# Optimization experiments

Hardware: AMD Instinct MI355X
Metric: run time of the kernel (lower is better)

## Reference

```python
import jax, jax.numpy as jnp
import numpy as np

# config (matches init_kwargs)
B, H, N, D = 2, 8, 2048, 64
ALPHA = 1.0        # < 2 -> power-law kernel branch
D_INT = 4.0        # d_intrinsic
BW = 1.0           # bandwidth
A = 0.5            # dual-sided degree-normalization exponent
R = 1.0            # sphere_radius
MASK_VAL = 10000.0
EPS = 1e-7


def setup_inputs() -> dict:
    key = jax.random.key(0)
    k1, k2, k3, k4 = jax.random.split(key, 4)
    Q = jax.random.normal(k1, (B, H, N, D), dtype=jnp.float32)
    K = jax.random.normal(k2, (B, H, N, D), dtype=jnp.float32)
    V = jax.random.normal(k3, (B, H, N, D), dtype=jnp.float32)
    mask = jax.random.randint(k4, (B, N), 0, 2).astype(jnp.int32)
    return {"Q": Q, "K": K, "V": V, "mask": mask}


def reference(Q, K, V, mask) -> jnp.ndarray:
    # geodesic distance on the sphere: acos(clamp(QK^T)) * radius  [B,H,N,N]
    qk = jnp.einsum('bhnd,bhmd->bhnm', Q, K)
    g_dist = jnp.arccos(jnp.clip(qk, -1.0 + EPS, 1.0 - EPS)) * R
    # key-side padding mask: [B,N] -> [B,1,1,N]
    g_dist = jnp.where(mask[:, None, None, :] == 0, MASK_VAL, g_dist)
    # power-law kernel (alpha < 2 branch)
    attn_score = (1.0 + g_dist / jnp.sqrt(BW)) ** (-D_INT - ALPHA)
    # dual-sided degree normalization (a != 0 branch)
    n_r = jnp.sum(attn_score, axis=-1)   # row degrees [B,H,N]
    n_c = jnp.sum(attn_score, axis=-2)   # col degrees [B,H,N]
    k_tilde = (n_r ** (-A))[..., :, None] * attn_score * (n_c ** (-A))[..., None, :]
    # F.normalize(p=1, dim=3)
    attn = k_tilde / jnp.maximum(jnp.sum(jnp.abs(k_tilde), axis=-1, keepdims=True), 1e-12)
    # dropout p=0.0 -> identity
    return jnp.einsum('bhnm,bhmd->bhnd', attn, V)
```

## Files before the change

### kernel.cpp

```cpp
#include <hip/hip_runtime.h>
#include <hip/hip_bf16.h>
#include <math.h>

#define B_ 2
#define H_ 8
#define N_ 2048
#define D_ 64
#define BH_ 16
#define NT_ (N_/64)
#define LS 72
#define LSW (LS/2)

typedef __attribute__((ext_vector_type(8))) short short8;
typedef __attribute__((ext_vector_type(4))) float float4v;
typedef __attribute__((ext_vector_type(2))) float float2v;

__device__ __forceinline__ float2v splat2(float s){ float2v v; v.x=s; v.y=s; return v; }

__device__ __forceinline__ unsigned packbf2(float a, float b){
  __hip_bfloat162 h = __float22bfloat162_rn(make_float2(a, b));
  return *(unsigned*)&h;
}
__device__ __forceinline__ void split2(float a, float b, unsigned& hi, unsigned& lo){
  hi = packbf2(a, b);
  float ha = __uint_as_float(hi << 16);
  float hb = __uint_as_float(hi & 0xFFFF0000u);
  lo = packbf2(a - ha, b - hb);
}
__device__ __forceinline__ void load_split8(const float* p, short8& hi8, short8& lo8){
  float4v v0 = *(const float4v*)p;
  float4v v1 = *(const float4v*)(p + 4);
  unsigned h0,h1,h2,h3,l0,l1,l2,l3;
  split2(v0.x, v0.y, h0, l0);
  split2(v0.z, v0.w, h1, l1);
  split2(v1.x, v1.y, h2, l2);
  split2(v1.z, v1.w, h3, l3);
  unsigned ph[4] = {h0,h1,h2,h3};
  unsigned pl[4] = {l0,l1,l2,l3};
  hi8 = *(short8*)ph;
  lo8 = *(short8*)pl;
}

__device__ __forceinline__ float2v score2(float2v qk){
  float2v ax;
  ax.x = fminf(fabsf(qk.x), 1.0f - 1e-7f);
  ax.y = fminf(fabsf(qk.y), 1.0f - 1e-7f);
  float2v p = __builtin_elementwise_fma(
                __builtin_elementwise_fma(
                  __builtin_elementwise_fma(splat2(-0.0187293f), ax, splat2(0.0742610f)),
                  ax, splat2(-0.2121144f)),
                ax, splat2(1.5707288f));
  float2v u = __builtin_elementwise_fma(ax, splat2(-1.0f), splat2(1.0f));
  float2v t;
  t.x = __builtin_amdgcn_sqrtf(u.x);
  t.y = __builtin_amdgcn_sqrtf(u.y);
  float2v t2 = t * p;
  float2v gn = __builtin_elementwise_fma(t2, splat2(-1.0f), splat2(3.14159265358979f));
  float2v g;
  g.x = (qk.x >= 0.0f) ? t2.x : gn.x;
  g.y = (qk.y >= 0.0f) ? t2.y : gn.y;
  float2v w1 = g + splat2(1.0f);
  float2v w2 = w1 * w1;
  float2v w4 = w2 * w2;
  float2v w5 = w4 * w1;
  float2v r;
  r.x = __builtin_amdgcn_rcpf(w5.x);
  r.y = __builtin_amdgcn_rcpf(w5.y);
  return r;
}

__device__ __forceinline__ float score_fn_m(float qk, float masked){
  float ax = fminf(fabsf(qk), 1.0f - 1e-7f);
  float t  = __builtin_amdgcn_sqrtf(1.0f - ax);
  float p  = __builtin_fmaf(__builtin_fmaf(__builtin_fmaf(-0.0187293f, ax, 0.0742610f),
                                           ax, -0.2121144f), ax, 1.5707288f);
  float t2 = t * p;
  float g  = (qk >= 0.0f) ? t2 : (3.14159265358979f - t2);
  g = (masked != 0.0f) ? 10000.0f : g;
  float w1 = 1.0f + g;
  float w2 = w1*w1;
  float w4 = w2*w2;
  return __builtin_amdgcn_rcpf(w4*w1);
}

__global__ __launch_bounds__(256) void k0_split(
    const float* __restrict__ Q, const float* __restrict__ K,
    unsigned short* __restrict__ Qh, unsigned short* __restrict__ Ql,
    unsigned short* __restrict__ Kh, unsigned short* __restrict__ Kl)
{
  size_t i = (size_t)blockIdx.x*256 + threadIdx.x;
  const size_t tot = (size_t)BH_*N_*D_/8;
  const float* src; unsigned short *dh, *dl;
  if (i < tot){ src = Q; dh = Qh; dl = Ql; }
  else        { src = K; dh = Kh; dl = Kl; i -= tot; }
  short8 hi, lo;
  load_split8(src + i*8, hi, lo);
  *(short8*)&dh[i*8] = hi;
  *(short8*)&dl[i*8] = lo;
}

template<bool PRE>
__global__ __launch_bounds__(256) void k1_score(
    const float* __restrict__ Qf, const float* __restrict__ Kf,
    const unsigned short* __restrict__ Qh, const unsigned short* __restrict__ Ql,
    const unsigned short* __restrict__ Kh, const unsigned short* __restrict__ Kl,
    float* __restrict__ ncw, unsigned short* __restrict__ S)
{
  __shared__ float red[64*4];
  const int id = blockIdx.x;
  const int xcd = id & 7;
  const int r0 = id >> 3;
  const int kt = r0 & 31;
  const int grp = r0 >> 5;
  const int flat = grp*8 + xcd;
  const int bh = flat & 15;
  const int rz = flat >> 4;
  const int tid = threadIdx.x;
  const int wv = tid>>6, lane = tid&63, quad = lane>>4, l15 = lane&15;

  short8 khi[4][2], klo[4][2];
  if constexpr (PRE){
    #pragma unroll
    for (int s=0;s<4;++s){
      const size_t r = (size_t)(bh*N_ + kt*64 + s*16 + l15)*D_ + quad*8;
      khi[s][0] = *(const short8*)&Kh[r];
      khi[s][1] = *(const short8*)&Kh[r+32];
      klo[s][0] = *(const short8*)&Kl[r];
      klo[s][1] = *(const short8*)&Kl[r+32];
    }
  } else {
    #pragma unroll
    for (int s=0;s<4;++s){
      const float* kp = Kf + (size_t)(bh*N_ + kt*64 + s*16 + l15)*D_ + quad*8;
      load_split8(kp,      khi[s][0], klo[s][0]);
      load_split8(kp + 32, khi[s][1], klo[s][1]);
    }
  }

  float2v cs2[4][2];
  #pragma unroll
  for (int s=0;s<4;++s){ cs2[s][0] = splat2(0.f); cs2[s][1] = splat2(0.f); }

  const int iters = NT_/4;
  const int rt0 = rz*iters;

  const size_t qoff0 = (size_t)(bh*N_ + rt0*64 + wv*16 + l15)*D_ + quad*8;
  const unsigned lconst = (unsigned)(((quad>>1)<<7) + (l15<<3) + ((quad&1)<<2));
  unsigned short* Sp = S + ((((size_t)(bh*NT_ + kt)*NT_ + rt0)*4 + wv)<<10) + lconst;

  short8 qh0,qh1,ql0,ql1;
  if constexpr (PRE){
    const unsigned short* qp = Qh + qoff0;
    const unsigned short* lp = Ql + qoff0;
    qh0 = *(const short8*)qp;      qh1 = *(const short8*)(qp+32);
    ql0 = *(const short8*)lp;      ql1 = *(const short8*)(lp+32);
  } else {
    const float* qp = Qf + qoff0;
    load_split8(qp,      qh0, ql0);
    load_split8(qp + 32, qh1, ql1);
  }

  for (int rti=0; rti<iters; ++rti){
    short8 nh0,nh1,nl0,nl1;
    const size_t qoffn = qoff0 + (size_t)(rti + ((rti+1<iters) ? 1 : 0))*4096;
    if constexpr (PRE){
      const unsigned short* qp = Qh + qoffn;
      const unsigned short* lp = Ql + qoffn;
      nh0 = *(const short8*)qp;    nh1 = *(const short8*)(qp+32);
      nl0 = *(const short8*)lp;    nl1 = *(const short8*)(lp+32);
    } else {
      const float* qp = Qf + qoffn;
      load_split8(qp,      nh0, nl0);
      load_split8(qp + 32, nh1, nl1);
    }

    #pragma unroll
    for (int s=0;s<4;++s){
      float4v c = {0.f,0.f,0.f,0.f};
      c = __builtin_amdgcn_mfma_f32_16x16x32_bf16(khi[s][0], qh0, c, 0,0,0);
      c = __builtin_amdgcn_mfma_f32_16x16x32_bf16(khi[s][0], ql0, c, 0,0,0);
      c = __builtin_amdgcn_mfma_f32_16x16x32_bf16(klo[s][0], qh0, c, 0,0,0);
      c = __builtin_amdgcn_mfma_f32_16x16x32_bf16(khi[s][1], qh1, c, 0,0,0);
      c = __builtin_amdgcn_mfma_f32_16x16x32_bf16(khi[s][1], ql1, c, 0,0,0);
      c = __builtin_amdgcn_mfma_f32_16x16x32_bf16(klo[s][1], qh1, c, 0,0,0);
      float2v c01; c01.x = c[0]; c01.y = c[1];
      float2v c23; c23.x = c[2]; c23.y = c[3];
      float2v s01 = score2(c01);
      float2v s23 = score2(c23);
      cs2[s][0] += s01;
      cs2[s][1] += s23;
      uint2 pk;
      pk.x = packbf2(s01.x, s01.y);
      pk.y = packbf2(s23.x, s23.y);
      *(uint2*)(Sp + (s<<8)) = pk;
    }
    Sp += 4096;
    qh0=nh0; qh1=nh1; ql0=nl0; ql1=nl1;
  }

  float cs[4][4];
  #pragma unroll
  for (int s=0;s<4;++s){
    cs[s][0]=cs2[s][0].x; cs[s][1]=cs2[s][0].y;
    cs[s][2]=cs2[s][1].x; cs[s][3]=cs2[s][1].y;
  }

  #pragma unroll
  for (int s=0;s<4;++s)
    #pragma unroll
    for (int i=0;i<4;++i){
      float v2 = cs[s][i];
      v2 += __shfl_xor(v2, 1);
      v2 += __shfl_xor(v2, 2);
      v2 += __shfl_xor(v2, 4);
      v2 += __shfl_xor(v2, 8);
      cs[s][i] = v2;
    }
  if (l15 == 0){
    #pragma unroll
    for (int s=0;s<4;++s)
      #pragma unroll
      for (int i=0;i<4;++i)
        red[(s*16 + quad*4 + i)*4 + wv] = cs[s][i];
  }
  __syncthreads();
  if (tid < 64){
    float t = red[tid*4+0] + red[tid*4+1] + red[tid*4+2] + red[tid*4+3];
    atomicAdd(&ncw[bh*N_ + kt*64 + tid], t);
  }
}

__global__ __launch_bounds__(256) void k2_pack(
    const float* __restrict__ V, const float* __restrict__ nc,
    const int* __restrict__ mask, unsigned short* __restrict__ Vw)
{
  __shared__ float T[64*65];
  __shared__ float wrow[64];
  const int id = blockIdx.x;
  const int xcd = id & 7;
  const int r0 = id >> 3;
  const int bh = (r0 & 1)*8 + xcd;
  const int mt = r0 >> 1;
  const int tid = threadIdx.x;
  const float* Vg = V + (size_t)bh*N_*D_;
  const float* ncg = nc + (size_t)bh*N_;
  unsigned short* Fb = Vw + ((size_t)(bh*NT_ + mt)*10)*512;

  {
    int m = tid >> 2;
    int d0 = (tid & 3) * 16;
    int gm = mt*64 + m;
    float wm = (mask[(bh>>3)*N_ + gm] == 0) ? 0.0f
             : (1.0f / sqrtf(fmaxf(ncg[gm], 1e-30f)));
    if (d0 == 0) wrow[m] = wm;
    #pragma unroll
    for (int j=0;j<4;++j){
      float4v v = *(const float4v*)(Vg + (size_t)gm*D_ + d0 + j*4);
      T[(d0+j*4+0)*65 + m] = v.x*wm;
      T[(d0+j*4+1)*65 + m] = v.y*wm;
      T[(d0+j*4+2)*65 + m] = v.z*wm;
      T[(d0+j*4+3)*65 + m] = v.w*wm;
    }
  }
  __syncthreads();

  for (int idx = tid; idx < 640; idx += 256){
    int f = idx >> 6, lane = idx & 63;
    int quad = lane >> 4, l15 = lane & 15;
    int s2 = f >> 1, cc = f & 1;
    int m0 = cc*32 + quad*8;
    unsigned pk[4];
    if (s2 < 4){
      int d = s2*16 + l15;
      #pragma unroll
      for (int j=0;j<4;++j)
        pk[j] = packbf2(T[d*65 + m0 + 2*j], T[d*65 + m0 + 2*j + 1]);
    } else if (l15 == 0){
      #pragma unroll
      for (int j=0;j<4;++j)
        pk[j] = packbf2(wrow[m0 + 2*j], wrow[m0 + 2*j + 1]);
    } else {
      pk[0]=pk[1]=pk[2]=pk[3]=0u;
    }
    *(short8*)(Fb + ((size_t)f*64 + lane)*8) = *(short8*)pk;
  }
}

__global__ __launch_bounds__(1024) void k3_stage(
    const unsigned short* __restrict__ S, const unsigned short* __restrict__ Vw,
    float* __restrict__ out)
{
  __shared__ unsigned short Vs[2*2*10*512];

  const int id = blockIdx.x;
  const int xcd = id & 7;
  const int r0 = id >> 3;
  const int bh  = (r0 & 1)*8 + xcd;
  const int rtp = r0 >> 1;

  const int tid = threadIdx.x;
  const int wvid = tid >> 6;
  const int g    = wvid >> 3;
  const int slot = wvid & 7;
  const int lane = tid & 63, quad = lane >> 4, l15 = lane & 15;

  const int row = rtp*128 + slot*16 + l15;
  const int rt  = rtp*2 + (slot>>2);

  const size_t sb0 = ((((size_t)bh*NT_ + g*16)*NT_ + rt)*4 + (size_t)(slot&3))*1024
                   + (size_t)quad*128 + (size_t)l15*8;

  const int gg0 = (tid >= 640) ? 1 : 0;
  const int rem0 = tid - gg0*640;
  const int f0 = rem0 >> 6, ln0 = rem0 & 63;
  const bool has1 = (tid < 256);
  const int rem1 = tid + 384;
  const int f1 = rem1 >> 6, ln1 = rem1 & 63;
  const size_t vwbh = (size_t)bh*NT_;

  float4v acc[4];
  #pragma unroll
  for (int i=0;i<4;++i) acc[i] = (float4v){0.f,0.f,0.f,0.f};
  float4v c5 = {0.f,0.f,0.f,0.f};

  {
    short8 a = *(const short8*)&Vw[(((vwbh + gg0*16)*10 + f0) << 9) + ln0*8];
    *(short8*)&Vs[((gg0*10 + f0) << 9) + ln0*8] = a;
    if (has1){
      short8 b = *(const short8*)&Vw[(((vwbh + 16)*10 + f1) << 9) + ln1*8];
      *(short8*)&Vs[((1*10 + f1) << 9) + ln1*8] = b;
    }
  }
  short8 npf0 = *(const short8*)&S[sb0];
  short8 npf1 = *(const short8*)&S[sb0 + 512];
  __syncthreads();

  for (int it = 0; it < 16; ++it){
    const int cur = it & 1, nxt = cur ^ 1;
    short8 pf0 = npf0, pf1 = npf1;
    short8 vwa, vwb;
    if (it < 15){
      vwa = *(const short8*)&Vw[(((vwbh + (size_t)(gg0*16 + it + 1))*10 + f0) << 9) + ln0*8];
      if (has1)
        vwb = *(const short8*)&Vw[(((vwbh + (size_t)(16 + it + 1))*10 + f1) << 9) + ln1*8];
      const size_t sb = sb0 + (size_t)(it+1)*131072;
      npf0 = *(const short8*)&S[sb];
      npf1 = *(const short8*)&S[sb + 512];
    }

    const unsigned short* Fl = &Vs[((cur*2 + g)*10) << 9] + (size_t)lane*8;
    short8 va[10];
    #pragma unroll
    for (int f=0; f<10; ++f)
      va[f] = *(const short8*)(Fl + ((size_t)f << 9));

    #pragma unroll
    for (int s2=0;s2<4;++s2){
      acc[s2] = __builtin_amdgcn_mfma_f32_16x16x32_bf16(va[s2*2+0], pf0, acc[s2], 0,0,0);
      acc[s2] = __builtin_amdgcn_mfma_f32_16x16x32_bf16(va[s2*2+1], pf1, acc[s2], 0,0,0);
    }
    c5 = __builtin_amdgcn_mfma_f32_16x16x32_bf16(va[8], pf0, c5, 0,0,0);
    c5 = __builtin_amdgcn_mfma_f32_16x16x32_bf16(va[9], pf1, c5, 0,0,0);

    if (it < 15){
      *(short8*)&Vs[(((nxt*2 + gg0)*10 + f0) << 9) + ln0*8] = vwa;
      if (has1)
        *(short8*)&Vs[(((nxt*2 + 1)*10 + f1) << 9) + ln1*8] = vwb;
    }
    __syncthreads();
  }

  float* Red = (float*)Vs;
  if (g == 1){
    float* Rr = Red + (size_t)(slot*16 + l15)*68;
    #pragma unroll
    for (int s2=0;s2<4;++s2)
      #pragma unroll
      for (int i=0;i<4;++i)
        Rr[s2*16 + quad*4 + i] = acc[s2][i];
    if (quad == 0) Rr[64] = c5[0];
  }
  __syncthreads();
  if (g == 0){
    const float* Rr = Red + (size_t)(slot*16 + l15)*68;
    #pragma unroll
    for (int s2=0;s2<4;++s2)
      #pragma unroll
      for (int i=0;i<4;++i)
        acc[s2][i] += Rr[s2*16 + quad*4 + i];
    float rs = __shfl(c5[0], l15) + Rr[64];
    float inv = 1.0f / fmaxf(rs, 1e-12f);

    float* Og = out + (size_t)bh*N_*D_ + (size_t)row*D_;
    #pragma unroll
    for (int s2=0;s2<4;++s2)
      #pragma unroll
      for (int i=0;i<4;++i)
        Og[s2*16 + quad*4 + i] = acc[s2][i] * inv;
  }
}

__global__ __launch_bounds__(256) void k1_fallback(
    const float* __restrict__ Q, const float* __restrict__ K,
    const int* __restrict__ mask, float* __restrict__ ncw)
{
  __shared__ float msk[64];
  __shared__ float red[64*4];
  const int kt = blockIdx.x, bh = blockIdx.y;
  const int tid = threadIdx.x;
  const int wv = tid>>6, lane = tid&63, quad = lane>>4, l15 = lane&15;

  const float* Qg = Q + (size_t)bh*N_*D_;
  const float* Kg = K + (size_t)bh*N_*D_;

  short8 khi[4][2], klo[4][2];
  #pragma unroll
  for (int s=0;s<4;++s){
    const float* kp = Kg + (size_t)(kt*64 + s*16 + l15)*D_ + quad*8;
    load_split8(kp,      khi[s][0], klo[s][0]);
    load_split8(kp + 32, khi[s][1], klo[s][1]);
  }
  if (tid < 64)
    msk[tid] = (mask[(bh>>3)*N_ + kt*64 + tid] == 0) ? 1.f : 0.f;
  __syncthreads();

  float cs[4][4];
  #pragma unroll
  for (int s=0;s<4;++s)
    #pragma unroll
    for (int i=0;i<4;++i) cs[s][i] = 0.f;

  for (int rt=0; rt<NT_; ++rt){
    const float* qp = Qg + (size_t)(rt*64 + wv*16 + l15)*D_ + quad*8;
    short8 bhi[2], blo[2];
    load_split8(qp,      bhi[0], blo[0]);
    load_split8(qp + 32, bhi[1], blo[1]);

    #pragma unroll
    for (int s=0;s<4;++s){
      float4v c = {0.f,0.f,0.f,0.f};
      #pragma unroll
      for (int cc=0; cc<2; ++cc){
        c = __builtin_amdgcn_mfma_f32_16x16x32_bf16(khi[s][cc], bhi[cc], c, 0,0,0);
        c = __builtin_amdgcn_mfma_f32_16x16x32_bf16(khi[s][cc], blo[cc], c, 0,0,0);
        c = __builtin_amdgcn_mfma_f32_16x16x32_bf16(klo[s][cc], bhi[cc], c, 0,0,0);
      }
      int kl = s*16 + quad*4;
      cs[s][0] += score_fn_m(c[0], msk[kl+0]);
      cs[s][1] += score_fn_m(c[1], msk[kl+1]);
      cs[s][2] += score_fn_m(c[2], msk[kl+2]);
      cs[s][3] += score_fn_m(c[3], msk[kl+3]);
    }
  }

  #pragma unroll
  for (int s=0;s<4;++s)
    #pragma unroll
    for (int i=0;i<4;++i){
      float v2 = cs[s][i];
      v2 += __shfl_xor(v2, 1);
      v2 += __shfl_xor(v2, 2);
      v2 += __shfl_xor(v2, 4);
      v2 += __shfl_xor(v2, 8);
      cs[s][i] = v2;
    }
  if (l15 == 0){
    #pragma unroll
    for (int s=0;s<4;++s)
      #pragma unroll
      for (int i=0;i<4;++i)
        red[(s*16 + quad*4 + i)*4 + wv] = cs[s][i];
  }
  __syncthreads();
  if (tid < 64){
    float t = red[tid*4+0] + red[tid*4+1] + red[tid*4+2] + red[tid*4+3];
    ncw[bh*N_ + kt*64 + tid] = 1.0f / sqrtf(t);
  }
}

__global__ __launch_bounds__(256) void spop_pass2(
    const float* __restrict__ Q, const float* __restrict__ K,
    const float* __restrict__ V, const int* __restrict__ mask,
    const float* __restrict__ w, float* __restrict__ out)
{
  __shared__ unsigned short Khi[64*LS], Klo[64*LS];
  __shared__ unsigned short Vt[64*LS];
  __shared__ unsigned short Ps[64*LS];
  __shared__ float msk[64], wms[64];

  const int rt = blockIdx.x, bh = blockIdx.y, b = bh>>3;
  const int tid = threadIdx.x;
  const int wv = tid>>6, lane = tid&63, quad = lane>>4, l15 = lane&15;

  const float* Qg = Q + (size_t)bh*N_*D_;
  const float* Kg = K + (size_t)bh*N_*D_;
  const float* Vg = V + (size_t)bh*N_*D_;

  short8 qhi[2], qlo[2];
  {
    const float* qp = Qg + (size_t)(rt*64 + wv*16 + l15)*D_ + quad*8;
    load_split8(qp,      qhi[0], qlo[0]);
    load_split8(qp + 32, qhi[1], qlo[1]);
  }

  float4v acc[4];
  #pragma unroll
  for (int i=0;i<4;++i) acc[i] = (float4v){0.f,0.f,0.f,0.f};
  float rs = 0.f;

  for (int kt=0; kt<NT_; ++kt){
    __syncthreads();
    #pragma unroll
    for (int it=0; it<4; ++it){
      int idx = tid + it*256;
      int r = idx>>4, d4 = (idx&15)<<2;
      const float4v v = *(const float4v*)(Kg + (size_t)(kt*64 + r)*D_ + d4);
      unsigned h0,l0,h1,l1;
      split2(v.x, v.y, h0, l0);
      split2(v.z, v.w, h1, l1);
      unsigned* KhiW = (unsigned*)Khi; unsigned* KloW = (unsigned*)Klo;
      int base = r*LSW + (d4>>1);
      KhiW[base] = h0; KhiW[base+1] = h1;
      KloW[base] = l0; KloW[base+1] = l1;
    }
    #pragma unroll
    for (int it=0; it<2; ++it){
      int u = tid + it*256;
      int kp = u & 31;
      int d4 = (u>>5)<<2;
      const float* vp = Vg + (size_t)(kt*64 + kp*2)*D_ + d4;
      float4v a0 = *(const float4v*)vp;
      float4v a1 = *(const float4v*)(vp + D_);
      unsigned* VtW = (unsigned*)Vt;
      VtW[(d4+0)*LSW + kp] = packbf2(a0.x, a1.x);
      VtW[(d4+1)*LSW + kp] = packbf2(a0.y, a1.y);
      VtW[(d4+2)*LSW + kp] = packbf2(a0.z, a1.z);
      VtW[(d4+3)*LSW + kp] = packbf2(a0.w, a1.w);
    }
    if (tid < 64){
      int gk = kt*64 + tid;
      msk[tid] = (mask[b*N_ + gk] == 0) ? 1.f : 0.f;
      wms[tid] = w[bh*N_ + gk];
    }
    __syncthreads();

    #pragma unroll
    for (int s=0;s<4;++s){
      float4v c = {0.f,0.f,0.f,0.f};
      #pragma unroll
      for (int cc=0; cc<2; ++cc){
        const short8 ahi = *(const short8*)&Khi[(s*16+l15)*LS + cc*32 + quad*8];
        const short8 alo = *(const short8*)&Klo[(s*16+l15)*LS + cc*32 + quad*8];
        c = __builtin_amdgcn_mfma_f32_16x16x32_bf16(ahi, qhi[cc], c, 0,0,0);
        c = __builtin_amdgcn_mfma_f32_16x16x32_bf16(ahi, qlo[cc], c, 0,0,0);
        c = __builtin_amdgcn_mfma_f32_16x16x32_bf16(alo, qhi[cc], c, 0,0,0);
      }
      int kl = s*16 + quad*4;
      float sc0 = score_fn_m(c[0], msk[kl+0]) * wms[kl+0];
      float sc1 = score_fn_m(c[1], msk[kl+1]) * wms[kl+1];
      float sc2 = score_fn_m(c[2], msk[kl+2]) * wms[kl+2];
      float sc3 = score_fn_m(c[3], msk[kl+3]) * wms[kl+3];
      rs += (sc0 + sc1) + (sc2 + sc3);
      unsigned* PsW = (unsigned*)Ps;
      int pb = (wv*16 + l15)*LSW + (kl>>1);
      PsW[pb]   = packbf2(sc0, sc1);
      PsW[pb+1] = packbf2(sc2, sc3);
    }

    short8 pf[2];
    pf[0] = *(const short8*)&Ps[(wv*16+l15)*LS +  0 + quad*8];
    pf[1] = *(const short8*)&Ps[(wv*16+l15)*LS + 32 + quad*8];
    #pragma unroll
    for (int s2=0;s2<4;++s2){
      #pragma unroll
      for (int cc=0; cc<2; ++cc){
        const short8 av = *(const short8*)&Vt[(s2*16+l15)*LS + cc*32 + quad*8];
        acc[s2] = __builtin_amdgcn_mfma_f32_16x16x32_bf16(av, pf[cc], acc[s2], 0,0,0);
      }
    }
  }

  rs += __shfl_xor(rs, 16);
  rs += __shfl_xor(rs, 32);
  float inv = 1.0f / fmaxf(rs, 1e-12f);

  float* Og = out + (size_t)bh*N_*D_ + (size_t)(rt*64 + wv*16 + l15)*D_;
  #pragma unroll
  for (int s2=0;s2<4;++s2)
    #pragma unroll
    for (int i=0;i<4;++i)
      Og[s2*16 + quad*4 + i] = acc[s2][i] * inv;
}

extern "C" void kernel_launch(void* const* d_in, const int* in_sizes, int n_in,
                              void* d_out, int out_size, void* d_ws, size_t ws_size,
                              hipStream_t stream) {
  (void)in_sizes; (void)n_in; (void)out_size;
  const float* Q   = (const float*)d_in[0];
  const float* K   = (const float*)d_in[1];
  const float* V   = (const float*)d_in[2];
  const int*  mask = (const int*)d_in[3];
  float* out = (float*)d_out;

  const size_t nc_bytes = (size_t)BH_*N_*sizeof(float);
  const size_t vw_off   = 131072;
  const size_t vw_bytes = (size_t)BH_*NT_*10*512*2;
  const size_t qk_off   = vw_off + vw_bytes;
  const size_t qk_one   = (size_t)BH_*N_*D_;
  const size_t qk_bytes = 4*qk_one*2;
  const size_t S_bytes  = (size_t)2*BH_*N_*N_;
  const size_t need_A   = qk_off + qk_bytes + S_bytes;
  const size_t need_B   = qk_off + S_bytes;

  if (ws_size >= need_A){
    float* nc = (float*)d_ws;
    unsigned short* Vw = (unsigned short*)((char*)d_ws + vw_off);
    unsigned short* Qh = (unsigned short*)((char*)d_ws + qk_off);
    unsigned short* Ql = Qh + qk_one;
    unsigned short* Kh = Ql + qk_one;
    unsigned short* Kl = Kh + qk_one;
    unsigned short* S  = (unsigned short*)((char*)d_ws + qk_off + qk_bytes);
    hipMemsetAsync(nc, 0, nc_bytes, stream);
    k0_split<<<dim3(2048), 256, 0, stream>>>(Q, K, Qh, Ql, Kh, Kl);
    k1_score<true><<<dim3(2048), 256, 0, stream>>>(
        nullptr, nullptr, Qh, Ql, Kh, Kl, nc, S);
    k2_pack<<<dim3(512), 256, 0, stream>>>(V, nc, mask, Vw);
    k3_stage<<<dim3(256), 1024, 0, stream>>>(S, Vw, out);
  } else if (ws_size >= need_B){
    float* nc = (float*)d_ws;
    unsigned short* Vw = (unsigned short*)((char*)d_ws + vw_off);
    unsigned short* S  = (unsigned short*)((char*)d_ws + qk_off);
    hipMemsetAsync(nc, 0, nc_bytes, stream);
    k1_score<false><<<dim3(2048), 256, 0, stream>>>(
        Q, K, nullptr, nullptr, nullptr, nullptr, nc, S);
    k2_pack<<<dim3(512), 256, 0, stream>>>(V, nc, mask, Vw);
    k3_stage<<<dim3(256), 1024, 0, stream>>>(S, Vw, out);
  } else {
    float* w = (float*)d_ws;
    k1_fallback<<<dim3(NT_, BH_), 256, 0, stream>>>(Q, K, mask, w);
    spop_pass2<<<dim3(NT_, BH_), 256, 0, stream>>>(Q, K, V, mask, w, out);
  }
}
```

Measured before the change: 164.3 us.

## Split MFMA accumulation chains and deepen S prefetch with unrolled double-buffer loop

In the QK score loop, the six dependent MFMAs per tile are split into two independent accumulator chains that are summed at the end, which shortens the dependency latency. In the PV loop, the iteration is manually unrolled by two with static LDS buffer indices, and the S tile prefetch is extended to two iterations ahead using two register sets. This is meant to hide global load latency and remove per-iteration buffer index arithmetic, at the cost of more live registers and a possible drop in occupancy.

```diff
diff --git a/kernel.cpp b/kernel.cpp
--- a/kernel.cpp
+++ b/kernel.cpp
@@ -176,13 +176,15 @@
 
     #pragma unroll
     for (int s=0;s<4;++s){
-      float4v c = {0.f,0.f,0.f,0.f};
-      c = __builtin_amdgcn_mfma_f32_16x16x32_bf16(khi[s][0], qh0, c, 0,0,0);
-      c = __builtin_amdgcn_mfma_f32_16x16x32_bf16(khi[s][0], ql0, c, 0,0,0);
-      c = __builtin_amdgcn_mfma_f32_16x16x32_bf16(klo[s][0], qh0, c, 0,0,0);
-      c = __builtin_amdgcn_mfma_f32_16x16x32_bf16(khi[s][1], qh1, c, 0,0,0);
-      c = __builtin_amdgcn_mfma_f32_16x16x32_bf16(khi[s][1], ql1, c, 0,0,0);
-      c = __builtin_amdgcn_mfma_f32_16x16x32_bf16(klo[s][1], qh1, c, 0,0,0);
+      float4v ca = {0.f,0.f,0.f,0.f};
+      float4v cb = {0.f,0.f,0.f,0.f};
+      ca = __builtin_amdgcn_mfma_f32_16x16x32_bf16(khi[s][0], qh0, ca, 0,0,0);
+      cb = __builtin_amdgcn_mfma_f32_16x16x32_bf16(khi[s][1], qh1, cb, 0,0,0);
+      ca = __builtin_amdgcn_mfma_f32_16x16x32_bf16(khi[s][0], ql0, ca, 0,0,0);
+      cb = __builtin_amdgcn_mfma_f32_16x16x32_bf16(khi[s][1], ql1, cb, 0,0,0);
+      ca = __builtin_amdgcn_mfma_f32_16x16x32_bf16(klo[s][0], qh0, ca, 0,0,0);
+      cb = __builtin_amdgcn_mfma_f32_16x16x32_bf16(klo[s][1], qh1, cb, 0,0,0);
+      float4v c = ca + cb;
       float2v c01; c01.x = c[0]; c01.y = c[1];
       float2v c23; c23.x = c[2]; c23.y = c[3];
       float2v s01 = score2(c01);
@@ -331,43 +333,84 @@
       *(short8*)&Vs[((1*10 + f1) << 9) + ln1*8] = b;
     }
   }
-  short8 npf0 = *(const short8*)&S[sb0];
-  short8 npf1 = *(const short8*)&S[sb0 + 512];
+  short8 sA0 = *(const short8*)&S[sb0];
+  short8 sA1 = *(const short8*)&S[sb0 + 512];
+  short8 sB0 = *(const short8*)&S[sb0 + 131072];
+  short8 sB1 = *(const short8*)&S[sb0 + 131072 + 512];
   __syncthreads();
 
-  for (int it = 0; it < 16; ++it){
-    const int cur = it & 1, nxt = cur ^ 1;
-    short8 pf0 = npf0, pf1 = npf1;
-    short8 vwa, vwb;
-    if (it < 15){
-      vwa = *(const short8*)&Vw[(((vwbh + (size_t)(gg0*16 + it + 1))*10 + f0) << 9) + ln0*8];
+  #pragma unroll 1
+  for (int k2 = 0; k2 < 8; ++k2){
+    const int itA = k2*2, itB = k2*2 + 1;
+
+    {
+      short8 vwa, vwb;
+      vwa = *(const short8*)&Vw[(((vwbh + (size_t)(gg0*16 + itA + 1))*10 + f0) << 9) + ln0*8];
       if (has1)
-        vwb = *(const short8*)&Vw[(((vwbh + (size_t)(16 + it + 1))*10 + f1) << 9) + ln1*8];
-      const size_t sb = sb0 + (size_t)(it+1)*131072;
-      npf0 = *(const short8*)&S[sb];
-      npf1 = *(const short8*)&S[sb + 512];
-    }
-
-    const unsigned short* Fl = &Vs[((cur*2 + g)*10) << 9] + (size_t)lane*8;
-    short8 va[10];
-    #pragma unroll
-    for (int f=0; f<10; ++f)
-      va[f] = *(const short8*)(Fl + ((size_t)f << 9));
-
-    #pragma unroll
-    for (int s2=0;s2<4;++s2){
-      acc[s2] = __builtin_amdgcn_mfma_f32_16x16x32_bf16(va[s2*2+0], pf0, acc[s2], 0,0,0);
-      acc[s2] = __builtin_amdgcn_mfma_f32_16x16x32_bf16(va[s2*2+1], pf1, acc[s2], 0,0,0);
-    }
-    c5 = __builtin_amdgcn_mfma_f32_16x16x32_bf16(va[8], pf0, c5, 0,0,0);
-    c5 = __builtin_amdgcn_mfma_f32_16x16x32_bf16(va[9], pf1, c5, 0,0,0);
-
-    if (it < 15){
-      *(short8*)&Vs[(((nxt*2 + gg0)*10 + f0) << 9) + ln0*8] = vwa;
+        vwb = *(const short8*)&Vw[(((vwbh + (size_t)(16 + itA + 1))*10 + f1) << 9) + ln1*8];
+      short8 p0 = sA0, p1 = sA1;
+      if (itA + 2 < 16){
+        const size_t sb = sb0 + (size_t)(itA+2)*131072;
+        sA0 = *(const short8*)&S[sb];
+        sA1 = *(const short8*)&S[sb + 512];
+      }
+
+      const unsigned short* Fl = &Vs[((0*2 + g)*10) << 9] + (size_t)lane*8;
+      short8 va[10];
+      #pragma unroll
+      for (int f=0; f<10; ++f)
+        va[f] = *(const short8*)(Fl + ((size_t)f << 9));
+
+      #pragma unroll
+      for (int s2=0;s2<4;++s2){
+        acc[s2] = __builtin_amdgcn_mfma_f32_16x16x32_bf16(va[s2*2+0], p0, acc[s2], 0,0,0);
+        acc[s2] = __builtin_amdgcn_mfma_f32_16x16x32_bf16(va[s2*2+1], p1, acc[s2], 0,0,0);
+      }
+      c5 = __builtin_amdgcn_mfma_f32_16x16x32_bf16(va[8], p0, c5, 0,0,0);
+      c5 = __builtin_amdgcn_mfma_f32_16x16x32_bf16(va[9], p1, c5, 0,0,0);
+
+      *(short8*)&Vs[(((1*2 + gg0)*10 + f0) << 9) + ln0*8] = vwa;
       if (has1)
-        *(short8*)&Vs[(((nxt*2 + 1)*10 + f1) << 9) + ln1*8] = vwb;
-    }
-    __syncthreads();
+        *(short8*)&Vs[(((1*2 + 1)*10 + f1) << 9) + ln1*8] = vwb;
+      __syncthreads();
+    }
+
+    {
+      short8 vwa, vwb;
+      const bool stage = (itB + 1 < 16);
+      if (stage){
+        vwa = *(const short8*)&Vw[(((vwbh + (size_t)(gg0*16 + itB + 1))*10 + f0) << 9) + ln0*8];
+        if (has1)
+          vwb = *(const short8*)&Vw[(((vwbh + (size_t)(16 + itB + 1))*10 + f1) << 9) + ln1*8];
+      }
+      short8 p0 = sB0, p1 = sB1;
+      if (itB + 2 < 16){
+        const size_t sb = sb0 + (size_t)(itB+2)*131072;
+        sB0 = *(const short8*)&S[sb];
+        sB1 = *(const short8*)&S[sb + 512];
+      }
+
+      const unsigned short* Fl = &Vs[((1*2 + g)*10) << 9] + (size_t)lane*8;
+      short8 va[10];
+      #pragma unroll
+      for (int f=0; f<10; ++f)
+        va[f] = *(const short8*)(Fl + ((size_t)f << 9));
+
+      #pragma unroll
+      for (int s2=0;s2<4;++s2){
+        acc[s2] = __builtin_amdgcn_mfma_f32_16x16x32_bf16(va[s2*2+0], p0, acc[s2], 0,0,0);
+        acc[s2] = __builtin_amdgcn_mfma_f32_16x16x32_bf16(va[s2*2+1], p1, acc[s2], 0,0,0);
+      }
+      c5 = __builtin_amdgcn_mfma_f32_16x16x32_bf16(va[8], p0, c5, 0,0,0);
+      c5 = __builtin_amdgcn_mfma_f32_16x16x32_bf16(va[9], p1, c5, 0,0,0);
+
+      if (stage){
+        *(short8*)&Vs[(((0*2 + gg0)*10 + f0) << 9) + ln0*8] = vwa;
+        if (has1)
+          *(short8*)&Vs[(((0*2 + 1)*10 + f1) << 9) + ln1*8] = vwb;
+      }
+      __syncthreads();
+    }
   }
 
   float* Red = (float*)Vs;
```

Result: no change. 165.2 us (+0.5%).

## Split MFMA accumulation chains and halve k3 block size to 512 threads

Applied to the files above, without the earlier changes.

In the score kernel, the six dependent MFMAs per sub-tile are split into two independent accumulator chains that are summed at the end, which shortens the MFMA dependency latency. The final PV kernel now runs 512 blocks of 512 threads, each covering a 64-row tile instead of a 128-row pair. The V-staging loads are redistributed across the smaller thread count. This gives more, smaller workgroups for better CU scheduling, at the cost of each block reloading the full V panel and so doubling V traffic into shared memory.

```diff
diff --git a/kernel.cpp b/kernel.cpp
--- a/kernel.cpp
+++ b/kernel.cpp
@@ -176,13 +176,15 @@
 
     #pragma unroll
     for (int s=0;s<4;++s){
-      float4v c = {0.f,0.f,0.f,0.f};
-      c = __builtin_amdgcn_mfma_f32_16x16x32_bf16(khi[s][0], qh0, c, 0,0,0);
-      c = __builtin_amdgcn_mfma_f32_16x16x32_bf16(khi[s][0], ql0, c, 0,0,0);
-      c = __builtin_amdgcn_mfma_f32_16x16x32_bf16(klo[s][0], qh0, c, 0,0,0);
-      c = __builtin_amdgcn_mfma_f32_16x16x32_bf16(khi[s][1], qh1, c, 0,0,0);
-      c = __builtin_amdgcn_mfma_f32_16x16x32_bf16(khi[s][1], ql1, c, 0,0,0);
-      c = __builtin_amdgcn_mfma_f32_16x16x32_bf16(klo[s][1], qh1, c, 0,0,0);
+      float4v ca = {0.f,0.f,0.f,0.f};
+      float4v cb = {0.f,0.f,0.f,0.f};
+      ca = __builtin_amdgcn_mfma_f32_16x16x32_bf16(khi[s][0], qh0, ca, 0,0,0);
+      cb = __builtin_amdgcn_mfma_f32_16x16x32_bf16(khi[s][1], qh1, cb, 0,0,0);
+      ca = __builtin_amdgcn_mfma_f32_16x16x32_bf16(khi[s][0], ql0, ca, 0,0,0);
+      cb = __builtin_amdgcn_mfma_f32_16x16x32_bf16(khi[s][1], ql1, cb, 0,0,0);
+      ca = __builtin_amdgcn_mfma_f32_16x16x32_bf16(klo[s][0], qh0, ca, 0,0,0);
+      cb = __builtin_amdgcn_mfma_f32_16x16x32_bf16(klo[s][1], qh1, cb, 0,0,0);
+      float4v c = ca + cb;
       float2v c01; c01.x = c[0]; c01.y = c[1];
       float2v c23; c23.x = c[2]; c23.y = c[3];
       float2v s01 = score2(c01);
@@ -286,7 +288,7 @@
   }
 }
 
-__global__ __launch_bounds__(1024) void k3_stage(
+__global__ __launch_bounds__(512) void k3_stage(
     const unsigned short* __restrict__ S, const unsigned short* __restrict__ Vw,
     float* __restrict__ out)
 {
@@ -295,27 +297,28 @@
   const int id = blockIdx.x;
   const int xcd = id & 7;
   const int r0 = id >> 3;
-  const int bh  = (r0 & 1)*8 + xcd;
-  const int rtp = r0 >> 1;
+  const int rt = r0 & 31;
+  const int bhh = r0 >> 5;
+  const int bh = bhh*8 + xcd;
 
   const int tid = threadIdx.x;
   const int wvid = tid >> 6;
-  const int g    = wvid >> 3;
-  const int slot = wvid & 7;
+  const int g    = wvid >> 2;
+  const int slot = wvid & 3;
   const int lane = tid & 63, quad = lane >> 4, l15 = lane & 15;
-
-  const int row = rtp*128 + slot*16 + l15;
-  const int rt  = rtp*2 + (slot>>2);
-
-  const size_t sb0 = ((((size_t)bh*NT_ + g*16)*NT_ + rt)*4 + (size_t)(slot&3))*1024
+  const int row = rt*64 + slot*16 + l15;
+
+  const size_t sb0 = ((((size_t)bh*NT_ + g*16)*NT_ + rt)*4 + (size_t)slot)*1024
                    + (size_t)quad*128 + (size_t)l15*8;
 
-  const int gg0 = (tid >= 640) ? 1 : 0;
-  const int rem0 = tid - gg0*640;
-  const int f0 = rem0 >> 6, ln0 = rem0 & 63;
-  const bool has1 = (tid < 256);
-  const int rem1 = tid + 384;
+  const int g0f = tid >> 6, g0ln = tid & 63;
+  const int c1 = tid + 512;
+  const int gg1 = (c1 >= 640) ? 1 : 0;
+  const int rem1 = c1 - gg1*640;
   const int f1 = rem1 >> 6, ln1 = rem1 & 63;
+  const bool has2 = (tid < 256);
+  const int rem2 = tid + 384;
+  const int f2 = rem2 >> 6, ln2 = rem2 & 63;
   const size_t vwbh = (size_t)bh*NT_;
 
   float4v acc[4];
@@ -324,11 +327,13 @@
   float4v c5 = {0.f,0.f,0.f,0.f};
 
   {
-    short8 a = *(const short8*)&Vw[(((vwbh + gg0*16)*10 + f0) << 9) + ln0*8];
-    *(short8*)&Vs[((gg0*10 + f0) << 9) + ln0*8] = a;
-    if (has1){
-      short8 b = *(const short8*)&Vw[(((vwbh + 16)*10 + f1) << 9) + ln1*8];
-      *(short8*)&Vs[((1*10 + f1) << 9) + ln1*8] = b;
+    short8 a = *(const short8*)&Vw[(vwbh + 0)*5120 + (size_t)g0f*512 + g0ln*8];
+    *(short8*)&Vs[((0*2 + 0)*10 + g0f)*512 + g0ln*8] = a;
+    short8 b = *(const short8*)&Vw[(vwbh + (size_t)gg1*16)*5120 + (size_t)f1*512 + ln1*8];
+    *(short8*)&Vs[((0*2 + gg1)*10 + f1)*512 + ln1*8] = b;
+    if (has2){
+      short8 c = *(const short8*)&Vw[(vwbh + 16)*5120 + (size_t)f2*512 + ln2*8];
+      *(short8*)&Vs[((0*2 + 1)*10 + f2)*512 + ln2*8] = c;
     }
   }
   short8 npf0 = *(const short8*)&S[sb0];
@@ -338,11 +343,12 @@
   for (int it = 0; it < 16; ++it){
     const int cur = it & 1, nxt = cur ^ 1;
     short8 pf0 = npf0, pf1 = npf1;
-    short8 vwa, vwb;
+    short8 vwa, vwb, vwc;
     if (it < 15){
-      vwa = *(const short8*)&Vw[(((vwbh + (size_t)(gg0*16 + it + 1))*10 + f0) << 9) + ln0*8];
-      if (has1)
-        vwb = *(const short8*)&Vw[(((vwbh + (size_t)(16 + it + 1))*10 + f1) << 9) + ln1*8];
+      vwa = *(const short8*)&Vw[(vwbh + (size_t)(it + 1))*5120 + (size_t)g0f*512 + g0ln*8];
+      vwb = *(const short8*)&Vw[(vwbh + (size_t)(gg1*16 + it + 1))*5120 + (size_t)f1*512 + ln1*8];
+      if (has2)
+        vwc = *(const short8*)&Vw[(vwbh + (size_t)(16 + it + 1))*5120 + (size_t)f2*512 + ln2*8];
       const size_t sb = sb0 + (size_t)(it+1)*131072;
       npf0 = *(const short8*)&S[sb];
       npf1 = *(const short8*)&S[sb + 512];
@@ -363,9 +369,10 @@
     c5 = __builtin_amdgcn_mfma_f32_16x16x32_bf16(va[9], pf1, c5, 0,0,0);
 
     if (it < 15){
-      *(short8*)&Vs[(((nxt*2 + gg0)*10 + f0) << 9) + ln0*8] = vwa;
-      if (has1)
-        *(short8*)&Vs[(((nxt*2 + 1)*10 + f1) << 9) + ln1*8] = vwb;
+      *(short8*)&Vs[((nxt*2 + 0)*10 + g0f)*512 + g0ln*8] = vwa;
+      *(short8*)&Vs[((nxt*2 + gg1)*10 + f1)*512 + ln1*8] = vwb;
+      if (has2)
+        *(short8*)&Vs[((nxt*2 + 1)*10 + f2)*512 + ln2*8] = vwc;
     }
     __syncthreads();
   }
@@ -625,7 +632,7 @@
     k1_score<true><<<dim3(2048), 256, 0, stream>>>(
         nullptr, nullptr, Qh, Ql, Kh, Kl, nc, S);
     k2_pack<<<dim3(512), 256, 0, stream>>>(V, nc, mask, Vw);
-    k3_stage<<<dim3(256), 1024, 0, stream>>>(S, Vw, out);
+    k3_stage<<<dim3(512), 512, 0, stream>>>(S, Vw, out);
   } else if (ws_size >= need_B){
     float* nc = (float*)d_ws;
     unsigned short* Vw = (unsigned short*)((char*)d_ws + vw_off);
@@ -634,7 +641,7 @@
     k1_score<false><<<dim3(2048), 256, 0, stream>>>(
         Q, K, nullptr, nullptr, nullptr, nullptr, nc, S);
     k2_pack<<<dim3(512), 256, 0, stream>>>(V, nc, mask, Vw);
-    k3_stage<<<dim3(256), 1024, 0, stream>>>(S, Vw, out);
+    k3_stage<<<dim3(512), 512, 0, stream>>>(S, Vw, out);
   } else {
     float* w = (float*)d_ws;
     k1_fallback<<<dim3(NT_, BH_), 256, 0, stream>>>(Q, K, mask, w);
```

Result: no change. 164.1 us (-0.1%).
